# Optimization experiments

Hardware: AMD Instinct MI355X
Metric: run time of the kernel (lower is better)

## Reference

```python
import jax, jax.numpy as jnp
import numpy as np

N, C, A = 8192, 1000, 768

def setup_inputs() -> dict:
    key = jax.random.key(0)
    k1, k2, k3, k4, k5 = jax.random.split(key, 5)
    return {
        "fc_weight": jax.random.normal(k1, (C, A), dtype=jnp.float32) * 0.02,
        "features": jax.random.normal(k2, (N, A), dtype=jnp.float32),
        "logits": jax.random.normal(k3, (N, C), dtype=jnp.float32),
        "labels": jax.random.randint(k4, (N,), 0, C, dtype=jnp.int64),
        "ratio": jnp.float32(0.5),
        "cv_matrix": jax.random.uniform(k5, (C, A), dtype=jnp.float32),
        "manner": 0,
    }

def reference(fc_weight, features, logits, labels, ratio, cv_matrix, manner):
    # fc_weight: [C, A]; logits: [N, C]; labels: [N]; cv_matrix: [C, A]
    n = features.shape[0]
    W = fc_weight
    Wk = W[labels]           # [N, A] gathered rows for each sample's label
    cvk = cv_matrix[labels]  # [N, A] per-sample diagonal covariance
    # sigma2[n, c] = ratio * sum_a (W[c,a] - Wk[n,a])^2 * cvk[n,a]
    # expanded to avoid the [N, C, A] intermediate:
    t1 = jnp.einsum('ca,na->nc', W * W, cvk)        # sum_a W^2 * cv
    t2 = jnp.einsum('ca,na->nc', W, Wk * cvk)       # sum_a W * Wk * cv
    t3 = jnp.sum(Wk * Wk * cvk, axis=1, keepdims=True)  # sum_a Wk^2 * cv
    sigma2 = ratio * (t1 - 2.0 * t2 + t3)
    aug_logits = logits + 0.5 * sigma2
    logp = jax.nn.log_softmax(aug_logits, axis=-1)
    loss = -jnp.mean(logp[jnp.arange(n), labels])
    return loss
```

## Files before the change

### kernel.cpp

```cpp
#include <hip/hip_runtime.h>
#include <cstdint>
#include <cstddef>

#define N_SAMPLES 8192
#define N_CLASSES 1000
#define C_PAD     1024
#define A_DIM     768
#define K_DIM     1536
#define BT 64
#define BK 64
#define NT (K_DIM / BK)

typedef __attribute__((ext_vector_type(8))) __bf16 bf16x8;
typedef __attribute__((ext_vector_type(4))) __bf16 bf16x4;
typedef __attribute__((ext_vector_type(4))) float  f32x4;

#define WAIT_VM(N) do { asm volatile("s_waitcnt vmcnt(" #N ")" ::: "memory"); \
                        __builtin_amdgcn_sched_barrier(0); } while (0)
#define WAIT_LGKM0 do { asm volatile("s_waitcnt lgkmcnt(0)" ::: "memory"); \
                        __builtin_amdgcn_sched_barrier(0); } while (0)

__global__ void prep(const float* __restrict__ W, const float* __restrict__ CV,
                     __bf16* __restrict__ UVc, __bf16* __restrict__ Wcat) {
    int gw   = (blockIdx.x * blockDim.x + threadIdx.x) >> 6;
    int lane = threadIdx.x & 63;
    bf16x4 z = {(__bf16)0.f, (__bf16)0.f, (__bf16)0.f, (__bf16)0.f};
    if (gw < C_PAD) {
        int l = gw;
        if (l < N_CLASSES) {
            #pragma unroll
            for (int p = 0; p < 3; ++p) {
                int a = p * 256 + lane * 4;
                f32x4 wk = *reinterpret_cast<const f32x4*>(W  + (size_t)l * A_DIM + a);
                f32x4 cv = *reinterpret_cast<const f32x4*>(CV + (size_t)l * A_DIM + a);
                bf16x4 u, v;
                #pragma unroll
                for (int j = 0; j < 4; ++j) {
                    u[j] = (__bf16)cv[j];
                    v[j] = (__bf16)(-2.0f * wk[j] * cv[j]);
                }
                *reinterpret_cast<bf16x4*>(UVc + (size_t)l * K_DIM + a)         = u;
                *reinterpret_cast<bf16x4*>(UVc + (size_t)l * K_DIM + A_DIM + a) = v;
            }
        } else {
            #pragma unroll
            for (int p = 0; p < 6; ++p)
                *reinterpret_cast<bf16x4*>(UVc + (size_t)l * K_DIM + p * 256 + lane * 4) = z;
        }
    } else {
        int c = gw - C_PAD;
        if (c < N_CLASSES) {
            #pragma unroll
            for (int p = 0; p < 3; ++p) {
                int a = p * 256 + lane * 4;
                f32x4 w = *reinterpret_cast<const f32x4*>(W + (size_t)c * A_DIM + a);
                bf16x4 sq, li;
                #pragma unroll
                for (int j = 0; j < 4; ++j) { sq[j] = (__bf16)(w[j] * w[j]); li[j] = (__bf16)w[j]; }
                *reinterpret_cast<bf16x4*>(Wcat + (size_t)c * K_DIM + a)         = sq;
                *reinterpret_cast<bf16x4*>(Wcat + (size_t)c * K_DIM + A_DIM + a) = li;
            }
        } else {
            #pragma unroll
            for (int p = 0; p < 6; ++p)
                *reinterpret_cast<bf16x4*>(Wcat + (size_t)c * K_DIM + p * 256 + lane * 4) = z;
        }
    }
}

__global__ __launch_bounds__(512, 2) void gemm_g(
        const __bf16* __restrict__ UVc, const __bf16* __restrict__ Wcat,
        __bf16* __restrict__ G) {
    __shared__ __align__(16) __bf16 As[3][BT * BK];
    __shared__ __align__(16) __bf16 Bs[3][BT * BK];
    int tid  = threadIdx.x;
    int lane = tid & 63;
    int wave = tid >> 6;
    int wgid = (blockIdx.x & 7) * 32 + (blockIdx.x >> 3);
    int rowBase = (wgid >> 4) * BT;
    int colBase = (wgid & 15) * BT;
    int wr = wave >> 1;
    int wc = wave & 1;

    f32x4 acc[2];
    acc[0] = (f32x4){0.f, 0.f, 0.f, 0.f};
    acc[1] = (f32x4){0.f, 0.f, 0.f, 0.f};

    auto stageA = [&](int b, int k0) {
        int row  = tid >> 3;
        int scch = (tid & 7) ^ (row & 7);
        int base = tid & ~63;
        const __bf16* ga = UVc + (size_t)(rowBase + row) * K_DIM + k0 + scch * 8;
        __builtin_amdgcn_global_load_lds(
            (const __attribute__((address_space(1))) void*)ga,
            (__attribute__((address_space(3))) void*)((char*)&As[b][0] + (size_t)base * 16),
            16, 0, 0);
    };
    auto stageB = [&](int b, int k0) {
        int row  = tid >> 3;
        int scch = (tid & 7) ^ (row & 7);
        int base = tid & ~63;
        const __bf16* gb = Wcat + (size_t)(colBase + row) * K_DIM + k0 + scch * 8;
        __builtin_amdgcn_global_load_lds(
            (const __attribute__((address_space(1))) void*)gb,
            (__attribute__((address_space(3))) void*)((char*)&Bs[b][0] + (size_t)base * 16),
            16, 0, 0);
    };
    auto loadFrags = [&](int b, int kk, bf16x8* af, bf16x8* bf) {
        int swch = ((kk * 4 + (lane >> 4)) ^ (lane & 7)) * 8;
        int r = wr * 16 + (lane & 15);
        af[0] = *reinterpret_cast<const bf16x8*>(&As[b][r * BK + swch]);
        #pragma unroll
        for (int n = 0; n < 2; ++n) {
            int c = wc * 32 + n * 16 + (lane & 15);
            bf[n] = *reinterpret_cast<const bf16x8*>(&Bs[b][c * BK + swch]);
        }
    };
    auto doMFMA = [&](bf16x8* af, bf16x8* bf) {
        __builtin_amdgcn_s_setprio(1);
        #pragma unroll
        for (int n = 0; n < 2; ++n)
            acc[n] = __builtin_amdgcn_mfma_f32_16x16x32_bf16(
                af[0], bf[n], acc[n], 0, 0, 0);
        __builtin_amdgcn_s_setprio(0);
    };

    stageA(0, 0);        stageB(0, 0);
    stageA(1, BK);       stageB(1, BK);
    WAIT_VM(2);
    __builtin_amdgcn_s_barrier();

    for (int kt = 0; kt < NT; ++kt) {
        int bR = kt % 3;
        int bS = (kt + 2) % 3;
        bool st = (kt + 2) < NT;
        int k2 = (kt + 2) * BK;
        bf16x8 af[1], bf[2];
        loadFrags(bR, 0, af, bf);
        if (st) stageA(bS, k2);
        __builtin_amdgcn_s_barrier();
        WAIT_LGKM0;
        doMFMA(af, bf);
        __builtin_amdgcn_s_barrier();
        loadFrags(bR, 1, af, bf);
        if (st) stageB(bS, k2);
        if (st) { WAIT_VM(2); } else { WAIT_VM(0); }
        __builtin_amdgcn_s_barrier();
        WAIT_LGKM0;
        doMFMA(af, bf);
        __builtin_amdgcn_s_barrier();
    }

    int lr = (lane >> 4) * 4;
    int lc = lane & 15;
    #pragma unroll
    for (int n = 0; n < 2; ++n) {
        int gr0 = rowBase + wr * 16 + lr;
        int gc  = colBase + wc * 32 + n * 16 + lc;
        #pragma unroll
        for (int j = 0; j < 4; ++j)
            G[(size_t)(gr0 + j) * C_PAD + gc] = (__bf16)acc[n][j];
    }
}

__global__ void softmax_loss(const __bf16* __restrict__ G,
                             const float* __restrict__ logits,
                             const float* __restrict__ ratiop,
                             const int* __restrict__ labels,
                             float* __restrict__ rowloss) {
    int tid  = threadIdx.x;
    int lane = tid & 63;
    int wv   = tid >> 6;
    int gw   = blockIdx.x * 4 + wv;
    float h  = 0.5f * ratiop[0];
    int  lab = labels[gw];
    const __bf16* rowp = G + (size_t)lab * C_PAD;
    const float*  lrow = logits + (size_t)gw * N_CLASSES;

    bf16x8 v0 = *reinterpret_cast<const bf16x8*>(rowp + lane * 8);
    bf16x8 v1 = *reinterpret_cast<const bf16x8*>(rowp + 512 + lane * 8);
    f32x4 l0a = __builtin_nontemporal_load(reinterpret_cast<const f32x4*>(lrow + lane * 8));
    f32x4 l0b = __builtin_nontemporal_load(reinterpret_cast<const f32x4*>(lrow + lane * 8 + 4));
    f32x4 l1a = {0.f,0.f,0.f,0.f}, l1b = {0.f,0.f,0.f,0.f};
    if (lane < 61) {
        l1a = __builtin_nontemporal_load(reinterpret_cast<const f32x4*>(lrow + 512 + lane * 8));
        l1b = __builtin_nontemporal_load(reinterpret_cast<const f32x4*>(lrow + 512 + lane * 8 + 4));
    }
    float f[16];
    #pragma unroll
    for (int j = 0; j < 4; ++j) {
        f[j]     = l0a[j] + h * (float)v0[j];
        f[4 + j] = l0b[j] + h * (float)v0[4 + j];
    }
    #pragma unroll
    for (int j = 0; j < 4; ++j) {
        f[8 + j]  = (lane < 61) ? l1a[j] + h * (float)v1[j]     : -1e30f;
        f[12 + j] = (lane < 61) ? l1b[j] + h * (float)v1[4 + j] : -1e30f;
    }
    float m = -1e30f;
    #pragma unroll
    for (int j = 0; j < 16; ++j) m = fmaxf(m, f[j]);
    #pragma unroll
    for (int s = 32; s > 0; s >>= 1) m = fmaxf(m, __shfl_xor(m, s));
    float sum = 0.f;
    #pragma unroll
    for (int j = 0; j < 16; ++j) sum += __expf(f[j] - m);
    #pragma unroll
    for (int s = 32; s > 0; s >>= 1) sum += __shfl_xor(sum, s);
    if (lane == 0) {
        float tv = lrow[lab] + h * (float)rowp[lab];
        rowloss[gw] = logf(sum) + m - tv;
    }
}

__global__ void finalize(const float* __restrict__ rowloss, float* __restrict__ out) {
    int tid = threadIdx.x;
    float part = 0.f;
    #pragma unroll
    for (int i = 0; i < 8; ++i) part += rowloss[i * 1024 + tid];
    #pragma unroll
    for (int s = 32; s > 0; s >>= 1) part += __shfl_xor(part, s);
    __shared__ float tmp[16];
    int lane = tid & 63, wv = tid >> 6;
    if (lane == 0) tmp[wv] = part;
    __syncthreads();
    if (tid == 0) {
        float sum = 0.f;
        #pragma unroll
        for (int w = 0; w < 16; ++w) sum += tmp[w];
        out[0] = sum / (float)N_SAMPLES;
    }
}

extern "C" void kernel_launch(void* const* d_in, const int* in_sizes, int n_in,
                              void* d_out, int out_size, void* d_ws, size_t ws_size,
                              hipStream_t stream) {
    const float* W      = (const float*)d_in[0];
    const float* logits = (const float*)d_in[2];
    const int*   labels = (const int*)d_in[3];
    const float* ratio  = (const float*)d_in[4];
    const float* CV     = (const float*)d_in[5];

    char* ws = (char*)d_ws;
    __bf16* Wcat    = (__bf16*)(ws + 0);
    __bf16* UVc     = (__bf16*)(ws + 3145728);
    __bf16* G       = (__bf16*)(ws + 6291456);
    float*  rowloss = (float*) (ws + 8388608);

    prep<<<2 * C_PAD / 4, 256, 0, stream>>>(W, CV, UVc, Wcat);
    gemm_g<<<256, 512, 0, stream>>>(UVc, Wcat, G);
    softmax_loss<<<N_SAMPLES / 4, 256, 0, stream>>>(G, logits, ratio, labels, rowloss);
    finalize<<<1, 1024, 0, stream>>>(rowloss, (float*)d_out);
}
```

Measured before the change: 38.09 us.

## Fuse prep, GEMM, softmax loss and reduction into one cooperative kernel

Merges the four separate kernel launches into a single cooperative kernel with 256 blocks of 512 threads. Each phase is separated by grid.sync(): operand prep, bf16 MFMA GEMM, per-row softmax loss with a per-block partial sum, then a final reduction in block 0. The goal is to remove launch gaps and inter-kernel tails. The cost is that grid-wide barriers and a fixed 256-block grid now drive the softmax phase, giving it far fewer waves than the earlier 2048-block launch.

After: 134.4 us. 253% more time.

```diff
diff --git a/kernel.cpp b/kernel.cpp
--- a/kernel.cpp
+++ b/kernel.cpp
@@ -1,6 +1,9 @@
 #include <hip/hip_runtime.h>
+#include <hip/hip_cooperative_groups.h>
 #include <cstdint>
 #include <cstddef>
+
+namespace cg = cooperative_groups;
 
 #define N_SAMPLES 8192
 #define N_CLASSES 1000
@@ -20,215 +23,228 @@
 #define WAIT_LGKM0 do { asm volatile("s_waitcnt lgkmcnt(0)" ::: "memory"); \
                         __builtin_amdgcn_sched_barrier(0); } while (0)
 
-__global__ void prep(const float* __restrict__ W, const float* __restrict__ CV,
-                     __bf16* __restrict__ UVc, __bf16* __restrict__ Wcat) {
-    int gw   = (blockIdx.x * blockDim.x + threadIdx.x) >> 6;
-    int lane = threadIdx.x & 63;
-    bf16x4 z = {(__bf16)0.f, (__bf16)0.f, (__bf16)0.f, (__bf16)0.f};
-    if (gw < C_PAD) {
-        int l = gw;
-        if (l < N_CLASSES) {
-            #pragma unroll
-            for (int p = 0; p < 3; ++p) {
-                int a = p * 256 + lane * 4;
-                f32x4 wk = *reinterpret_cast<const f32x4*>(W  + (size_t)l * A_DIM + a);
-                f32x4 cv = *reinterpret_cast<const f32x4*>(CV + (size_t)l * A_DIM + a);
-                bf16x4 u, v;
-                #pragma unroll
-                for (int j = 0; j < 4; ++j) {
-                    u[j] = (__bf16)cv[j];
-                    v[j] = (__bf16)(-2.0f * wk[j] * cv[j]);
-                }
-                *reinterpret_cast<bf16x4*>(UVc + (size_t)l * K_DIM + a)         = u;
-                *reinterpret_cast<bf16x4*>(UVc + (size_t)l * K_DIM + A_DIM + a) = v;
-            }
-        } else {
-            #pragma unroll
-            for (int p = 0; p < 6; ++p)
-                *reinterpret_cast<bf16x4*>(UVc + (size_t)l * K_DIM + p * 256 + lane * 4) = z;
-        }
-    } else {
-        int c = gw - C_PAD;
-        if (c < N_CLASSES) {
-            #pragma unroll
-            for (int p = 0; p < 3; ++p) {
-                int a = p * 256 + lane * 4;
-                f32x4 w = *reinterpret_cast<const f32x4*>(W + (size_t)c * A_DIM + a);
-                bf16x4 sq, li;
-                #pragma unroll
-                for (int j = 0; j < 4; ++j) { sq[j] = (__bf16)(w[j] * w[j]); li[j] = (__bf16)w[j]; }
-                *reinterpret_cast<bf16x4*>(Wcat + (size_t)c * K_DIM + a)         = sq;
-                *reinterpret_cast<bf16x4*>(Wcat + (size_t)c * K_DIM + A_DIM + a) = li;
-            }
-        } else {
-            #pragma unroll
-            for (int p = 0; p < 6; ++p)
-                *reinterpret_cast<bf16x4*>(Wcat + (size_t)c * K_DIM + p * 256 + lane * 4) = z;
-        }
-    }
-}
-
-__global__ __launch_bounds__(512, 2) void gemm_g(
-        const __bf16* __restrict__ UVc, const __bf16* __restrict__ Wcat,
-        __bf16* __restrict__ G) {
+__global__ __launch_bounds__(512, 2) void fused_isda(
+        const float* __restrict__ W, const float* __restrict__ CV,
+        const float* __restrict__ logits, const int* __restrict__ labels,
+        const float* __restrict__ ratiop,
+        __bf16* __restrict__ UVc, __bf16* __restrict__ Wcat,
+        __bf16* __restrict__ G, float* __restrict__ partial,
+        float* __restrict__ out) {
     __shared__ __align__(16) __bf16 As[3][BT * BK];
     __shared__ __align__(16) __bf16 Bs[3][BT * BK];
+    __shared__ float red[8];
+    cg::grid_group grid = cg::this_grid();
+
     int tid  = threadIdx.x;
     int lane = tid & 63;
     int wave = tid >> 6;
-    int wgid = (blockIdx.x & 7) * 32 + (blockIdx.x >> 3);
-    int rowBase = (wgid >> 4) * BT;
-    int colBase = (wgid & 15) * BT;
-    int wr = wave >> 1;
-    int wc = wave & 1;
-
-    f32x4 acc[2];
-    acc[0] = (f32x4){0.f, 0.f, 0.f, 0.f};
-    acc[1] = (f32x4){0.f, 0.f, 0.f, 0.f};
-
-    auto stageA = [&](int b, int k0) {
-        int row  = tid >> 3;
-        int scch = (tid & 7) ^ (row & 7);
-        int base = tid & ~63;
-        const __bf16* ga = UVc + (size_t)(rowBase + row) * K_DIM + k0 + scch * 8;
-        __builtin_amdgcn_global_load_lds(
-            (const __attribute__((address_space(1))) void*)ga,
-            (__attribute__((address_space(3))) void*)((char*)&As[b][0] + (size_t)base * 16),
-            16, 0, 0);
-    };
-    auto stageB = [&](int b, int k0) {
-        int row  = tid >> 3;
-        int scch = (tid & 7) ^ (row & 7);
-        int base = tid & ~63;
-        const __bf16* gb = Wcat + (size_t)(colBase + row) * K_DIM + k0 + scch * 8;
-        __builtin_amdgcn_global_load_lds(
-            (const __attribute__((address_space(1))) void*)gb,
-            (__attribute__((address_space(3))) void*)((char*)&Bs[b][0] + (size_t)base * 16),
-            16, 0, 0);
-    };
-    auto loadFrags = [&](int b, int kk, bf16x8* af, bf16x8* bf) {
-        int swch = ((kk * 4 + (lane >> 4)) ^ (lane & 7)) * 8;
-        int r = wr * 16 + (lane & 15);
-        af[0] = *reinterpret_cast<const bf16x8*>(&As[b][r * BK + swch]);
+
+    {
+        int gw = blockIdx.x * 8 + wave;
+        bf16x4 z = {(__bf16)0.f, (__bf16)0.f, (__bf16)0.f, (__bf16)0.f};
+        if (gw < C_PAD) {
+            int l = gw;
+            if (l < N_CLASSES) {
+                #pragma unroll
+                for (int p = 0; p < 3; ++p) {
+                    int a = p * 256 + lane * 4;
+                    f32x4 wk = *reinterpret_cast<const f32x4*>(W  + (size_t)l * A_DIM + a);
+                    f32x4 cv = *reinterpret_cast<const f32x4*>(CV + (size_t)l * A_DIM + a);
+                    bf16x4 u, v;
+                    #pragma unroll
+                    for (int j = 0; j < 4; ++j) {
+                        u[j] = (__bf16)cv[j];
+                        v[j] = (__bf16)(-2.0f * wk[j] * cv[j]);
+                    }
+                    *reinterpret_cast<bf16x4*>(UVc + (size_t)l * K_DIM + a)         = u;
+                    *reinterpret_cast<bf16x4*>(UVc + (size_t)l * K_DIM + A_DIM + a) = v;
+                }
+            } else {
+                #pragma unroll
+                for (int p = 0; p < 6; ++p)
+                    *reinterpret_cast<bf16x4*>(UVc + (size_t)l * K_DIM + p * 256 + lane * 4) = z;
+            }
+        } else {
+            int c = gw - C_PAD;
+            if (c < N_CLASSES) {
+                #pragma unroll
+                for (int p = 0; p < 3; ++p) {
+                    int a = p * 256 + lane * 4;
+                    f32x4 w = *reinterpret_cast<const f32x4*>(W + (size_t)c * A_DIM + a);
+                    bf16x4 sq, li;
+                    #pragma unroll
+                    for (int j = 0; j < 4; ++j) { sq[j] = (__bf16)(w[j] * w[j]); li[j] = (__bf16)w[j]; }
+                    *reinterpret_cast<bf16x4*>(Wcat + (size_t)c * K_DIM + a)         = sq;
+                    *reinterpret_cast<bf16x4*>(Wcat + (size_t)c * K_DIM + A_DIM + a) = li;
+                }
+            } else {
+                #pragma unroll
+                for (int p = 0; p < 6; ++p)
+                    *reinterpret_cast<bf16x4*>(Wcat + (size_t)c * K_DIM + p * 256 + lane * 4) = z;
+            }
+        }
+    }
+    grid.sync();
+
+    {
+        int wgid = (blockIdx.x & 7) * 32 + (blockIdx.x >> 3);
+        int rowBase = (wgid >> 4) * BT;
+        int colBase = (wgid & 15) * BT;
+        int wr = wave >> 1;
+        int wc = wave & 1;
+
+        f32x4 acc[2];
+        acc[0] = (f32x4){0.f, 0.f, 0.f, 0.f};
+        acc[1] = (f32x4){0.f, 0.f, 0.f, 0.f};
+
+        auto stageA = [&](int b, int k0) {
+            int row  = tid >> 3;
+            int scch = (tid & 7) ^ (row & 7);
+            int base = tid & ~63;
+            const __bf16* ga = UVc + (size_t)(rowBase + row) * K_DIM + k0 + scch * 8;
+            __builtin_amdgcn_global_load_lds(
+                (const __attribute__((address_space(1))) void*)ga,
+                (__attribute__((address_space(3))) void*)((char*)&As[b][0] + (size_t)base * 16),
+                16, 0, 0);
+        };
+        auto stageB = [&](int b, int k0) {
+            int row  = tid >> 3;
+            int scch = (tid & 7) ^ (row & 7);
+            int base = tid & ~63;
+            const __bf16* gb = Wcat + (size_t)(colBase + row) * K_DIM + k0 + scch * 8;
+            __builtin_amdgcn_global_load_lds(
+                (const __attribute__((address_space(1))) void*)gb,
+                (__attribute__((address_space(3))) void*)((char*)&Bs[b][0] + (size_t)base * 16),
+                16, 0, 0);
+        };
+        auto loadFrags = [&](int b, int kk, bf16x8* af, bf16x8* bf) {
+            int swch = ((kk * 4 + (lane >> 4)) ^ (lane & 7)) * 8;
+            int r = wr * 16 + (lane & 15);
+            af[0] = *reinterpret_cast<const bf16x8*>(&As[b][r * BK + swch]);
+            #pragma unroll
+            for (int n = 0; n < 2; ++n) {
+                int c = wc * 32 + n * 16 + (lane & 15);
+                bf[n] = *reinterpret_cast<const bf16x8*>(&Bs[b][c * BK + swch]);
+            }
+        };
+        auto doMFMA = [&](bf16x8* af, bf16x8* bf) {
+            __builtin_amdgcn_s_setprio(1);
+            #pragma unroll
+            for (int n = 0; n < 2; ++n)
+                acc[n] = __builtin_amdgcn_mfma_f32_16x16x32_bf16(
+                    af[0], bf[n], acc[n], 0, 0, 0);
+            __builtin_amdgcn_s_setprio(0);
+        };
+
+        stageA(0, 0);        stageB(0, 0);
+        stageA(1, BK);       stageB(1, BK);
+        WAIT_VM(2);
+        __builtin_amdgcn_s_barrier();
+
+        for (int kt = 0; kt < NT; ++kt) {
+            int bR = kt % 3;
+            int bS = (kt + 2) % 3;
+            bool st = (kt + 2) < NT;
+            int k2 = (kt + 2) * BK;
+            bf16x8 af[1], bf[2];
+            loadFrags(bR, 0, af, bf);
+            if (st) stageA(bS, k2);
+            __builtin_amdgcn_s_barrier();
+            WAIT_LGKM0;
+            doMFMA(af, bf);
+            __builtin_amdgcn_s_barrier();
+            loadFrags(bR, 1, af, bf);
+            if (st) stageB(bS, k2);
+            if (st) { WAIT_VM(2); } else { WAIT_VM(0); }
+            __builtin_amdgcn_s_barrier();
+            WAIT_LGKM0;
+            doMFMA(af, bf);
+            __builtin_amdgcn_s_barrier();
+        }
+
+        int lr = (lane >> 4) * 4;
+        int lc = lane & 15;
         #pragma unroll
         for (int n = 0; n < 2; ++n) {
-            int c = wc * 32 + n * 16 + (lane & 15);
-            bf[n] = *reinterpret_cast<const bf16x8*>(&Bs[b][c * BK + swch]);
-        }
-    };
-    auto doMFMA = [&](bf16x8* af, bf16x8* bf) {
-        __builtin_amdgcn_s_setprio(1);
+            int gr0 = rowBase + wr * 16 + lr;
+            int gc  = colBase + wc * 32 + n * 16 + lc;
+            #pragma unroll
+            for (int j = 0; j < 4; ++j)
+                G[(size_t)(gr0 + j) * C_PAD + gc] = (__bf16)acc[n][j];
+        }
+    }
+    grid.sync();
+
+    {
+        float h = 0.5f * ratiop[0];
+        float wloss = 0.f;
         #pragma unroll
-        for (int n = 0; n < 2; ++n)
-            acc[n] = __builtin_amdgcn_mfma_f32_16x16x32_bf16(
-                af[0], bf[n], acc[n], 0, 0, 0);
-        __builtin_amdgcn_s_setprio(0);
-    };
-
-    stageA(0, 0);        stageB(0, 0);
-    stageA(1, BK);       stageB(1, BK);
-    WAIT_VM(2);
-    __builtin_amdgcn_s_barrier();
-
-    for (int kt = 0; kt < NT; ++kt) {
-        int bR = kt % 3;
-        int bS = (kt + 2) % 3;
-        bool st = (kt + 2) < NT;
-        int k2 = (kt + 2) * BK;
-        bf16x8 af[1], bf[2];
-        loadFrags(bR, 0, af, bf);
-        if (st) stageA(bS, k2);
-        __builtin_amdgcn_s_barrier();
-        WAIT_LGKM0;
-        doMFMA(af, bf);
-        __builtin_amdgcn_s_barrier();
-        loadFrags(bR, 1, af, bf);
-        if (st) stageB(bS, k2);
-        if (st) { WAIT_VM(2); } else { WAIT_VM(0); }
-        __builtin_amdgcn_s_barrier();
-        WAIT_LGKM0;
-        doMFMA(af, bf);
-        __builtin_amdgcn_s_barrier();
-    }
-
-    int lr = (lane >> 4) * 4;
-    int lc = lane & 15;
-    #pragma unroll
-    for (int n = 0; n < 2; ++n) {
-        int gr0 = rowBase + wr * 16 + lr;
-        int gc  = colBase + wc * 32 + n * 16 + lc;
+        for (int it = 0; it < 4; ++it) {
+            int gw = blockIdx.x * 8 + wave + it * 2048;
+            int lab = labels[gw];
+            const __bf16* rowp = G + (size_t)lab * C_PAD;
+            const float*  lrow = logits + (size_t)gw * N_CLASSES;
+
+            bf16x8 v0 = *reinterpret_cast<const bf16x8*>(rowp + lane * 8);
+            bf16x8 v1 = *reinterpret_cast<const bf16x8*>(rowp + 512 + lane * 8);
+            f32x4 l0a = __builtin_nontemporal_load(reinterpret_cast<const f32x4*>(lrow + lane * 8));
+            f32x4 l0b = __builtin_nontemporal_load(reinterpret_cast<const f32x4*>(lrow + lane * 8 + 4));
+            f32x4 l1a = {0.f,0.f,0.f,0.f}, l1b = {0.f,0.f,0.f,0.f};
+            if (lane < 61) {
+                l1a = __builtin_nontemporal_load(reinterpret_cast<const f32x4*>(lrow + 512 + lane * 8));
+                l1b = __builtin_nontemporal_load(reinterpret_cast<const f32x4*>(lrow + 512 + lane * 8 + 4));
+            }
+            float f[16];
+            #pragma unroll
+            for (int j = 0; j < 4; ++j) {
+                f[j]     = l0a[j] + h * (float)v0[j];
+                f[4 + j] = l0b[j] + h * (float)v0[4 + j];
+            }
+            #pragma unroll
+            for (int j = 0; j < 4; ++j) {
+                f[8 + j]  = (lane < 61) ? l1a[j] + h * (float)v1[j]     : -1e30f;
+                f[12 + j] = (lane < 61) ? l1b[j] + h * (float)v1[4 + j] : -1e30f;
+            }
+            float m = -1e30f;
+            #pragma unroll
+            for (int j = 0; j < 16; ++j) m = fmaxf(m, f[j]);
+            #pragma unroll
+            for (int s = 32; s > 0; s >>= 1) m = fmaxf(m, __shfl_xor(m, s));
+            float sum = 0.f;
+            #pragma unroll
+            for (int j = 0; j < 16; ++j) sum += __expf(f[j] - m);
+            #pragma unroll
+            for (int s = 32; s > 0; s >>= 1) sum += __shfl_xor(sum, s);
+            if (lane == 0) {
+                float tv = lrow[lab] + h * (float)rowp[lab];
+                wloss += logf(sum) + m - tv;
+            }
+        }
+        __syncthreads();
+        if (lane == 0) red[wave] = wloss;
+        __syncthreads();
+        if (tid == 0) {
+            float s = 0.f;
+            #pragma unroll
+            for (int w = 0; w < 8; ++w) s += red[w];
+            partial[blockIdx.x] = s;
+        }
+    }
+    grid.sync();
+
+    if (blockIdx.x == 0) {
+        float p = (tid < 256) ? partial[tid] : 0.f;
         #pragma unroll
-        for (int j = 0; j < 4; ++j)
-            G[(size_t)(gr0 + j) * C_PAD + gc] = (__bf16)acc[n][j];
-    }
-}
-
-__global__ void softmax_loss(const __bf16* __restrict__ G,
-                             const float* __restrict__ logits,
-                             const float* __restrict__ ratiop,
-                             const int* __restrict__ labels,
-                             float* __restrict__ rowloss) {
-    int tid  = threadIdx.x;
-    int lane = tid & 63;
-    int wv   = tid >> 6;
-    int gw   = blockIdx.x * 4 + wv;
-    float h  = 0.5f * ratiop[0];
-    int  lab = labels[gw];
-    const __bf16* rowp = G + (size_t)lab * C_PAD;
-    const float*  lrow = logits + (size_t)gw * N_CLASSES;
-
-    bf16x8 v0 = *reinterpret_cast<const bf16x8*>(rowp + lane * 8);
-    bf16x8 v1 = *reinterpret_cast<const bf16x8*>(rowp + 512 + lane * 8);
-    f32x4 l0a = __builtin_nontemporal_load(reinterpret_cast<const f32x4*>(lrow + lane * 8));
-    f32x4 l0b = __builtin_nontemporal_load(reinterpret_cast<const f32x4*>(lrow + lane * 8 + 4));
-    f32x4 l1a = {0.f,0.f,0.f,0.f}, l1b = {0.f,0.f,0.f,0.f};
-    if (lane < 61) {
-        l1a = __builtin_nontemporal_load(reinterpret_cast<const f32x4*>(lrow + 512 + lane * 8));
-        l1b = __builtin_nontemporal_load(reinterpret_cast<const f32x4*>(lrow + 512 + lane * 8 + 4));
-    }
-    float f[16];
-    #pragma unroll
-    for (int j = 0; j < 4; ++j) {
-        f[j]     = l0a[j] + h * (float)v0[j];
-        f[4 + j] = l0b[j] + h * (float)v0[4 + j];
-    }
-    #pragma unroll
-    for (int j = 0; j < 4; ++j) {
-        f[8 + j]  = (lane < 61) ? l1a[j] + h * (float)v1[j]     : -1e30f;
-        f[12 + j] = (lane < 61) ? l1b[j] + h * (float)v1[4 + j] : -1e30f;
-    }
-    float m = -1e30f;
-    #pragma unroll
-    for (int j = 0; j < 16; ++j) m = fmaxf(m, f[j]);
-    #pragma unroll
-    for (int s = 32; s > 0; s >>= 1) m = fmaxf(m, __shfl_xor(m, s));
-    float sum = 0.f;
-    #pragma unroll
-    for (int j = 0; j < 16; ++j) sum += __expf(f[j] - m);
-    #pragma unroll
-    for (int s = 32; s > 0; s >>= 1) sum += __shfl_xor(sum, s);
-    if (lane == 0) {
-        float tv = lrow[lab] + h * (float)rowp[lab];
-        rowloss[gw] = logf(sum) + m - tv;
-    }
-}
-
-__global__ void finalize(const float* __restrict__ rowloss, float* __restrict__ out) {
-    int tid = threadIdx.x;
-    float part = 0.f;
-    #pragma unroll
-    for (int i = 0; i < 8; ++i) part += rowloss[i * 1024 + tid];
-    #pragma unroll
-    for (int s = 32; s > 0; s >>= 1) part += __shfl_xor(part, s);
-    __shared__ float tmp[16];
-    int lane = tid & 63, wv = tid >> 6;
-    if (lane == 0) tmp[wv] = part;
-    __syncthreads();
-    if (tid == 0) {
-        float sum = 0.f;
-        #pragma unroll
-        for (int w = 0; w < 16; ++w) sum += tmp[w];
-        out[0] = sum / (float)N_SAMPLES;
+        for (int s = 32; s > 0; s >>= 1) p += __shfl_xor(p, s);
+        __syncthreads();
+        if (lane == 0) red[wave] = p;
+        __syncthreads();
+        if (tid == 0) {
+            float s = 0.f;
+            #pragma unroll
+            for (int w = 0; w < 8; ++w) s += red[w];
+            out[0] = s / (float)N_SAMPLES;
+        }
     }
 }
 
@@ -245,10 +261,12 @@
     __bf16* Wcat    = (__bf16*)(ws + 0);
     __bf16* UVc     = (__bf16*)(ws + 3145728);
     __bf16* G       = (__bf16*)(ws + 6291456);
-    float*  rowloss = (float*) (ws + 8388608);
-
-    prep<<<2 * C_PAD / 4, 256, 0, stream>>>(W, CV, UVc, Wcat);
-    gemm_g<<<256, 512, 0, stream>>>(UVc, Wcat, G);
-    softmax_loss<<<N_SAMPLES / 4, 256, 0, stream>>>(G, logits, ratio, labels, rowloss);
-    finalize<<<1, 1024, 0, stream>>>(rowloss, (float*)d_out);
+    float*  partial = (float*) (ws + 8388608);
+    float*  outp    = (float*)d_out;
+
+    void* args[] = { (void*)&W, (void*)&CV, (void*)&logits, (void*)&labels,
+                     (void*)&ratio, (void*)&UVc, (void*)&Wcat, (void*)&G,
+                     (void*)&partial, (void*)&outp };
+    hipLaunchCooperativeKernel((const void*)fused_isda, dim3(256), dim3(512),
+                               args, 0, stream);
 }
```

## Fuse bf16 prep into GEMM loads and replace finalize with atomic reduction

Applied to the files above, without the earlier changes.

Removes the separate prep kernel: the GEMM now reads fp32 W and CV directly, computes cv, -2·w·cv, w² and w on the fly, converts them to bf16, and writes them to a double-buffered LDS tile (replacing the triple-buffered async global-to-LDS copies). The finalize kernel is also removed, and each softmax block atomically adds its scaled partial loss into the output, which the GEMM zeroes first. This saves two launches and the workspace round trip. In exchange, the GEMM does extra fp32 loads and conversion work in its main loop with a shallower pipeline, and the float atomic summation order is nondeterministic.

After: 57.72 us. 1.52x slower.

```diff
diff --git a/kernel.cpp b/kernel.cpp
--- a/kernel.cpp
+++ b/kernel.cpp
@@ -12,99 +12,79 @@
 #define NT (K_DIM / BK)
 
 typedef __attribute__((ext_vector_type(8))) __bf16 bf16x8;
-typedef __attribute__((ext_vector_type(4))) __bf16 bf16x4;
 typedef __attribute__((ext_vector_type(4))) float  f32x4;
 
-#define WAIT_VM(N) do { asm volatile("s_waitcnt vmcnt(" #N ")" ::: "memory"); \
+#define WAIT_VM0   do { asm volatile("s_waitcnt vmcnt(0)" ::: "memory"); \
                         __builtin_amdgcn_sched_barrier(0); } while (0)
 #define WAIT_LGKM0 do { asm volatile("s_waitcnt lgkmcnt(0)" ::: "memory"); \
                         __builtin_amdgcn_sched_barrier(0); } while (0)
 
-__global__ void prep(const float* __restrict__ W, const float* __restrict__ CV,
-                     __bf16* __restrict__ UVc, __bf16* __restrict__ Wcat) {
-    int gw   = (blockIdx.x * blockDim.x + threadIdx.x) >> 6;
-    int lane = threadIdx.x & 63;
-    bf16x4 z = {(__bf16)0.f, (__bf16)0.f, (__bf16)0.f, (__bf16)0.f};
-    if (gw < C_PAD) {
-        int l = gw;
-        if (l < N_CLASSES) {
-            #pragma unroll
-            for (int p = 0; p < 3; ++p) {
-                int a = p * 256 + lane * 4;
-                f32x4 wk = *reinterpret_cast<const f32x4*>(W  + (size_t)l * A_DIM + a);
-                f32x4 cv = *reinterpret_cast<const f32x4*>(CV + (size_t)l * A_DIM + a);
-                bf16x4 u, v;
-                #pragma unroll
-                for (int j = 0; j < 4; ++j) {
-                    u[j] = (__bf16)cv[j];
-                    v[j] = (__bf16)(-2.0f * wk[j] * cv[j]);
-                }
-                *reinterpret_cast<bf16x4*>(UVc + (size_t)l * K_DIM + a)         = u;
-                *reinterpret_cast<bf16x4*>(UVc + (size_t)l * K_DIM + A_DIM + a) = v;
-            }
-        } else {
-            #pragma unroll
-            for (int p = 0; p < 6; ++p)
-                *reinterpret_cast<bf16x4*>(UVc + (size_t)l * K_DIM + p * 256 + lane * 4) = z;
-        }
-    } else {
-        int c = gw - C_PAD;
-        if (c < N_CLASSES) {
-            #pragma unroll
-            for (int p = 0; p < 3; ++p) {
-                int a = p * 256 + lane * 4;
-                f32x4 w = *reinterpret_cast<const f32x4*>(W + (size_t)c * A_DIM + a);
-                bf16x4 sq, li;
-                #pragma unroll
-                for (int j = 0; j < 4; ++j) { sq[j] = (__bf16)(w[j] * w[j]); li[j] = (__bf16)w[j]; }
-                *reinterpret_cast<bf16x4*>(Wcat + (size_t)c * K_DIM + a)         = sq;
-                *reinterpret_cast<bf16x4*>(Wcat + (size_t)c * K_DIM + A_DIM + a) = li;
-            }
-        } else {
-            #pragma unroll
-            for (int p = 0; p < 6; ++p)
-                *reinterpret_cast<bf16x4*>(Wcat + (size_t)c * K_DIM + p * 256 + lane * 4) = z;
-        }
-    }
-}
-
 __global__ __launch_bounds__(512, 2) void gemm_g(
-        const __bf16* __restrict__ UVc, const __bf16* __restrict__ Wcat,
-        __bf16* __restrict__ G) {
-    __shared__ __align__(16) __bf16 As[3][BT * BK];
-    __shared__ __align__(16) __bf16 Bs[3][BT * BK];
+        const float* __restrict__ W, const float* __restrict__ CV,
+        __bf16* __restrict__ G, float* __restrict__ out) {
+    __shared__ __align__(16) __bf16 As[2][BT * BK];
+    __shared__ __align__(16) __bf16 Bs[2][BT * BK];
     int tid  = threadIdx.x;
     int lane = tid & 63;
     int wave = tid >> 6;
+    if (blockIdx.x == 0 && tid == 0) out[0] = 0.f;
+
     int wgid = (blockIdx.x & 7) * 32 + (blockIdx.x >> 3);
     int rowBase = (wgid >> 4) * BT;
     int colBase = (wgid & 15) * BT;
     int wr = wave >> 1;
     int wc = wave & 1;
 
+    int row = tid >> 3;
+    int g   = tid & 7;
+    int wsoff = row * (BK * 2) + ((g ^ (row & 7)) * 16);
+    int rA = rowBase + row;
+    int rB = colBase + row;
+    bool vA = rA < N_CLASSES;
+    bool vB = rB < N_CLASSES;
+    int cA = vA ? rA : N_CLASSES - 1;
+    int cB = vB ? rB : N_CLASSES - 1;
+
     f32x4 acc[2];
     acc[0] = (f32x4){0.f, 0.f, 0.f, 0.f};
     acc[1] = (f32x4){0.f, 0.f, 0.f, 0.f};
 
-    auto stageA = [&](int b, int k0) {
-        int row  = tid >> 3;
-        int scch = (tid & 7) ^ (row & 7);
-        int base = tid & ~63;
-        const __bf16* ga = UVc + (size_t)(rowBase + row) * K_DIM + k0 + scch * 8;
-        __builtin_amdgcn_global_load_lds(
-            (const __attribute__((address_space(1))) void*)ga,
-            (__attribute__((address_space(3))) void*)((char*)&As[b][0] + (size_t)base * 16),
-            16, 0, 0);
+    f32x4 ra[2], rwA[2], rbW[2];
+    #pragma unroll
+    for (int i = 0; i < 2; ++i) {
+        ra[i] = (f32x4){0,0,0,0}; rwA[i] = (f32x4){0,0,0,0}; rbW[i] = (f32x4){0,0,0,0};
+    }
+
+    auto stageLoad = [&](int kt) {
+        bool half = kt >= 12;
+        int aoff = (half ? (kt - 12) : kt) * 64 + g * 8;
+        const float* cvp = CV + (size_t)cA * A_DIM + aoff;
+        ra[0] = *reinterpret_cast<const f32x4*>(cvp);
+        ra[1] = *reinterpret_cast<const f32x4*>(cvp + 4);
+        const float* wbp = W + (size_t)cB * A_DIM + aoff;
+        rbW[0] = *reinterpret_cast<const f32x4*>(wbp);
+        rbW[1] = *reinterpret_cast<const f32x4*>(wbp + 4);
+        if (half) {
+            const float* wap = W + (size_t)cA * A_DIM + aoff;
+            rwA[0] = *reinterpret_cast<const f32x4*>(wap);
+            rwA[1] = *reinterpret_cast<const f32x4*>(wap + 4);
+        }
     };
-    auto stageB = [&](int b, int k0) {
-        int row  = tid >> 3;
-        int scch = (tid & 7) ^ (row & 7);
-        int base = tid & ~63;
-        const __bf16* gb = Wcat + (size_t)(colBase + row) * K_DIM + k0 + scch * 8;
-        __builtin_amdgcn_global_load_lds(
-            (const __attribute__((address_space(1))) void*)gb,
-            (__attribute__((address_space(3))) void*)((char*)&Bs[b][0] + (size_t)base * 16),
-            16, 0, 0);
+    auto convWrite = [&](int kt, int b) {
+        bool half = kt >= 12;
+        bf16x8 av, bv;
+        #pragma unroll
+        for (int j = 0; j < 8; ++j) {
+            float cv = ra[j >> 2][j & 3];
+            float wa = rwA[j >> 2][j & 3];
+            float wb = rbW[j >> 2][j & 3];
+            float aval = half ? (-2.0f * wa * cv) : cv;
+            float bval = half ? wb : (wb * wb);
+            av[j] = vA ? (__bf16)aval : (__bf16)0.f;
+            bv[j] = vB ? (__bf16)bval : (__bf16)0.f;
+        }
+        *reinterpret_cast<bf16x8*>((char*)&As[b][0] + wsoff) = av;
+        *reinterpret_cast<bf16x8*>((char*)&Bs[b][0] + wsoff) = bv;
     };
     auto loadFrags = [&](int b, int kk, bf16x8* af, bf16x8* bf) {
         int swch = ((kk * 4 + (lane >> 4)) ^ (lane & 7)) * 8;
@@ -116,38 +96,32 @@
             bf[n] = *reinterpret_cast<const bf16x8*>(&Bs[b][c * BK + swch]);
         }
     };
-    auto doMFMA = [&](bf16x8* af, bf16x8* bf) {
+
+    stageLoad(0);
+    WAIT_VM0;
+    convWrite(0, 0);
+    WAIT_LGKM0;
+    __builtin_amdgcn_s_barrier();
+
+    for (int kt = 0; kt < NT; ++kt) {
+        int bR = kt & 1;
+        bool st = (kt + 1) < NT;
+        if (st) stageLoad(kt + 1);
+        bf16x8 af0[1], bf0[2], af1[1], bf1[2];
+        loadFrags(bR, 0, af0, bf0);
+        loadFrags(bR, 1, af1, bf1);
+        WAIT_LGKM0;
         __builtin_amdgcn_s_setprio(1);
-        #pragma unroll
-        for (int n = 0; n < 2; ++n)
-            acc[n] = __builtin_amdgcn_mfma_f32_16x16x32_bf16(
-                af[0], bf[n], acc[n], 0, 0, 0);
+        acc[0] = __builtin_amdgcn_mfma_f32_16x16x32_bf16(af0[0], bf0[0], acc[0], 0, 0, 0);
+        acc[1] = __builtin_amdgcn_mfma_f32_16x16x32_bf16(af0[0], bf0[1], acc[1], 0, 0, 0);
+        acc[0] = __builtin_amdgcn_mfma_f32_16x16x32_bf16(af1[0], bf1[0], acc[0], 0, 0, 0);
+        acc[1] = __builtin_amdgcn_mfma_f32_16x16x32_bf16(af1[0], bf1[1], acc[1], 0, 0, 0);
         __builtin_amdgcn_s_setprio(0);
-    };
-
-    stageA(0, 0);        stageB(0, 0);
-    stageA(1, BK);       stageB(1, BK);
-    WAIT_VM(2);
-    __builtin_amdgcn_s_barrier();
-
-    for (int kt = 0; kt < NT; ++kt) {
-        int bR = kt % 3;
-        int bS = (kt + 2) % 3;
-        bool st = (kt + 2) < NT;
-        int k2 = (kt + 2) * BK;
-        bf16x8 af[1], bf[2];
-        loadFrags(bR, 0, af, bf);
-        if (st) stageA(bS, k2);
-        __builtin_amdgcn_s_barrier();
+        if (st) {
+            WAIT_VM0;
+            convWrite(kt + 1, bR ^ 1);
+        }
         WAIT_LGKM0;
-        doMFMA(af, bf);
-        __builtin_amdgcn_s_barrier();
-        loadFrags(bR, 1, af, bf);
-        if (st) stageB(bS, k2);
-        if (st) { WAIT_VM(2); } else { WAIT_VM(0); }
-        __builtin_amdgcn_s_barrier();
-        WAIT_LGKM0;
-        doMFMA(af, bf);
         __builtin_amdgcn_s_barrier();
     }
 
@@ -167,7 +141,7 @@
                              const float* __restrict__ logits,
                              const float* __restrict__ ratiop,
                              const int* __restrict__ labels,
-                             float* __restrict__ rowloss) {
+                             float* __restrict__ out) {
     int tid  = threadIdx.x;
     int lane = tid & 63;
     int wv   = tid >> 6;
@@ -207,29 +181,15 @@
     for (int j = 0; j < 16; ++j) sum += __expf(f[j] - m);
     #pragma unroll
     for (int s = 32; s > 0; s >>= 1) sum += __shfl_xor(sum, s);
+
+    __shared__ float pr[4];
     if (lane == 0) {
         float tv = lrow[lab] + h * (float)rowp[lab];
-        rowloss[gw] = logf(sum) + m - tv;
-    }
-}
-
-__global__ void finalize(const float* __restrict__ rowloss, float* __restrict__ out) {
-    int tid = threadIdx.x;
-    float part = 0.f;
-    #pragma unroll
-    for (int i = 0; i < 8; ++i) part += rowloss[i * 1024 + tid];
-    #pragma unroll
-    for (int s = 32; s > 0; s >>= 1) part += __shfl_xor(part, s);
-    __shared__ float tmp[16];
-    int lane = tid & 63, wv = tid >> 6;
-    if (lane == 0) tmp[wv] = part;
+        pr[wv] = logf(sum) + m - tv;
+    }
     __syncthreads();
-    if (tid == 0) {
-        float sum = 0.f;
-        #pragma unroll
-        for (int w = 0; w < 16; ++w) sum += tmp[w];
-        out[0] = sum / (float)N_SAMPLES;
-    }
+    if (tid == 0)
+        atomicAdd(out, (pr[0] + pr[1] + pr[2] + pr[3]) * (1.0f / (float)N_SAMPLES));
 }
 
 extern "C" void kernel_launch(void* const* d_in, const int* in_sizes, int n_in,
@@ -241,14 +201,9 @@
     const float* ratio  = (const float*)d_in[4];
     const float* CV     = (const float*)d_in[5];
 
-    char* ws = (char*)d_ws;
-    __bf16* Wcat    = (__bf16*)(ws + 0);
-    __bf16* UVc     = (__bf16*)(ws + 3145728);
-    __bf16* G       = (__bf16*)(ws + 6291456);
-    float*  rowloss = (float*) (ws + 8388608);
-
-    prep<<<2 * C_PAD / 4, 256, 0, stream>>>(W, CV, UVc, Wcat);
-    gemm_g<<<256, 512, 0, stream>>>(UVc, Wcat, G);
-    softmax_loss<<<N_SAMPLES / 4, 256, 0, stream>>>(G, logits, ratio, labels, rowloss);
-    finalize<<<1, 1024, 0, stream>>>(rowloss, (float*)d_out);
+    __bf16* G = (__bf16*)d_ws;
+
+    gemm_g<<<256, 512, 0, stream>>>(W, CV, G, (float*)d_out);
+    softmax_loss<<<N_SAMPLES / 4, 256, 0, stream>>>(G, logits, ratio, labels,
+                                                    (float*)d_out);
 }
```
